# Kernel optimization log

Measured on AMD Instinct MI355X. Metric: run time of the kernel, lower is better.

## Reference

```python
import jax, jax.numpy as jnp
import numpy as np

N, E, W, H, NXF, NDF = 131072, 8, 128, 64, 10, 4
DX = 3 + 3 * 2 * NXF  # 63
DV = 3 + 3 * 2 * NDF  # 27
TEMP = 0.166667


def pe(x, degree):
    # positional encoding: [x, sin(2^i x), cos(2^i x)]
    y = jnp.concatenate([(2.0 ** i) * x for i in range(degree)], -1)
    return jnp.concatenate([x, jnp.sin(y), jnp.cos(y)], -1)


def setup_inputs() -> dict:
    key = jax.random.key(0)
    ks = jax.random.split(key, 8)
    s = 0.05
    return {
        'x': jax.random.normal(ks[0], (N, 6), jnp.float32),
        'W_enc': jax.random.normal(ks[1], (DX, W), jnp.float32) * s,
        'b_enc': jnp.zeros((W,), jnp.float32),
        'W_sh': jax.random.normal(ks[2], (E, W, W), jnp.float32) * s,
        'b_sh': jnp.zeros((E, W), jnp.float32),
        'w_sig': jax.random.normal(ks[3], (W,), jnp.float32) * s,
        'b_sig': jnp.zeros((1,), jnp.float32),
        'W_r1': jax.random.normal(ks[4], (E, W + DV, H), jnp.float32) * s,
        'b_r1': jnp.zeros((E, H), jnp.float32),
        'W_r2': jax.random.normal(ks[5], (E, H, 3), jnp.float32) * s,
        'b_r2': jnp.zeros((E, 3), jnp.float32),
    }


def reference(x, W_enc, b_enc, W_sh, b_sh, w_sig, b_sig, W_r1, b_r1, W_r2, b_r2):
    xyz = pe(x[:, :3], NXF)          # [N, 63]
    vd = pe(x[:, 3:6], NDF)          # [N, 27]
    y = jax.nn.relu(xyz @ W_enc + b_enc)  # encoding_xyz -> [N, W]
    # all shape experts at once: [N, E, W]
    shape_out = jax.nn.relu(jnp.einsum('nd,edh->neh', y, W_sh) + b_sh)
    # shared sigma head, softplus keeps sigma > 0: [N, E]
    sigmas = jax.nn.softplus(jnp.einsum('neh,h->ne', shape_out, w_sig) + b_sig)
    log_logits = jax.nn.log_softmax(jnp.log(sigmas + 1e-10) / TEMP, axis=-1)
    # gumbel-softmax (tau=1, torch default) with fixed noise key
    u = jax.random.uniform(jax.random.key(42), sigmas.shape, jnp.float32)
    g = -jnp.log(-jnp.log(u + 1e-20) + 1e-20)
    gates_soft = jax.nn.softmax(log_logits + g, axis=-1)
    index = jnp.argmax(gates_soft, axis=-1)  # [N]
    hard = jax.nn.one_hot(index, E, dtype=sigmas.dtype)
    # straight-through hard gates
    gates_hard = hard - jax.lax.stop_gradient(gates_soft) + gates_soft
    sigmas_pooled = jnp.take_along_axis(sigmas, index[:, None], axis=-1)  # [N, 1]
    # rgb experts: concat(shape_out_i, viewdir) -> MLP -> sigmoid rgb, gated sum
    vdb = jnp.broadcast_to(vd[:, None, :], (vd.shape[0], E, DV))
    inp = jnp.concatenate([shape_out, vdb], axis=-1)  # [N, E, W+27]
    h = jax.nn.relu(jnp.einsum('nec,ech->neh', inp, W_r1) + b_r1)
    rgb = jax.nn.sigmoid(jnp.einsum('neh,eho->neo', h, W_r2) + b_r2)  # [N, E, 3]
    rgbs = jnp.sum(rgb * gates_hard[:, :, None], axis=1)  # [N, 3]
    return jnp.concatenate([rgbs, sigmas_pooled], axis=-1)  # [N, 4]
```

## Files before the change

### kernel.cpp

```cpp
#include <hip/hip_runtime.h>
#include <hip/hip_bf16.h>


#define NPTS 131072
#define PT 64
#define NTH 256
#define NBLK (NPTS / PT)
#define INV2048 (1.0f / 2048.0f)

#define WS_ENC_H 0
#define WS_ENC_L 8192
#define WS_SH_H  16384
#define WS_SH_L  147456
#define WS_R1_H  278528

#define OFF_YH   0
#define OFF_B    17408
#define OFF_RED  38912
#define SMEM_SZ  47104

#define S_LIST(s) (*(int*)(smem + OFF_B + (s) * 336 + 320))
#define S_BID(p)  (*(int*)(smem + OFF_B + (p) * 336 + 324))
#define S_CNT(e)  (*(int*)(smem + OFF_B + (e) * 336 + 328))
#define S_OFF(e)  (*(int*)(smem + OFF_B + (e) * 336 + 332))

typedef __attribute__((ext_vector_type(8))) _Float16 f16x8;
typedef __attribute__((ext_vector_type(4))) _Float16 f16x4;
typedef __attribute__((ext_vector_type(4))) float f32x4;

#define MFMA(a, b, c) __builtin_amdgcn_mfma_f32_16x16x32_f16((a), (b), (c), 0, 0, 0)

__device__ __forceinline__ unsigned rotl32(unsigned x, int d) {
  return (x << d) | (x >> (32 - d));
}

__device__ __forceinline__ float gumbel_for(unsigned flat) {
  const unsigned k0 = 0u, k1 = 42u;
  const unsigned ks2 = k0 ^ k1 ^ 0x1BD11BDAu;
  unsigned x0 = 0u + k0;
  unsigned x1 = flat + k1;
#define TF_RND(r) { x0 += x1; x1 = rotl32(x1, r); x1 ^= x0; }
  TF_RND(13) TF_RND(15) TF_RND(26) TF_RND(6)
  x0 += k1;  x1 += ks2 + 1u;
  TF_RND(17) TF_RND(29) TF_RND(16) TF_RND(24)
  x0 += ks2; x1 += k0 + 2u;
  TF_RND(13) TF_RND(15) TF_RND(26) TF_RND(6)
  x0 += k0;  x1 += k1 + 3u;
  TF_RND(17) TF_RND(29) TF_RND(16) TF_RND(24)
  x0 += k1;  x1 += ks2 + 4u;
  TF_RND(13) TF_RND(15) TF_RND(26) TF_RND(6)
  x0 += ks2; x1 += k0 + 5u;
#undef TF_RND
  unsigned bits = x0 ^ x1;
  float u = __uint_as_float((bits >> 9) | 0x3f800000u) - 1.0f;
  return -logf(-logf(u + 1e-20f) + 1e-20f);
}

__global__ void prep_kernel(const float* __restrict__ W_enc,
                            const float* __restrict__ W_sh,
                            const float* __restrict__ W_r1,
                            _Float16* __restrict__ ws) {
  int idx = blockIdx.x * 256 + threadIdx.x;
  if (idx < 8192) {
    int tile = idx >> 9, r = idx & 511;
    int L = r >> 3, j = r & 7;
    int nt = tile >> 1, kt = tile & 1;
    int k = kt * 32 + (L >> 4) * 8 + j;
    int n = nt * 16 + (L & 15);
    float v = (k < 63) ? W_enc[k * 128 + n] : 0.0f;
    _Float16 h = (_Float16)v;
    ws[WS_ENC_H + idx] = h;
    ws[WS_ENC_L + idx] = (_Float16)((v - (float)h) * 2048.0f);
  } else if (idx < 8192 + 131072) {
    int s = idx - 8192;
    int tile = s >> 9, r = s & 511;
    int L = r >> 3, j = r & 7;
    int e = tile >> 5, nt = (tile >> 2) & 7, kt = tile & 3;
    int k = kt * 32 + (L >> 4) * 8 + j;
    int n = nt * 16 + (L & 15);
    float v = W_sh[e * 16384 + k * 128 + n];
    _Float16 h = (_Float16)v;
    ws[WS_SH_H + s] = h;
    ws[WS_SH_L + s] = (_Float16)((v - (float)h) * 2048.0f);
  } else if (idx < 8192 + 131072 + 81920) {
    int s = idx - (8192 + 131072);
    int tile = s >> 9, r = s & 511;
    int L = r >> 3, j = r & 7;
    int e = tile / 20, rr = tile % 20;
    int nt = rr / 5, kt = rr % 5;
    int k = kt * 32 + (L >> 4) * 8 + j;
    int n = nt * 16 + (L & 15);
    float v = (k < 155) ? W_r1[e * 9920 + k * 64 + n] : 0.0f;
    ws[WS_R1_H + s] = (_Float16)v;
  }
}

__global__ __launch_bounds__(NTH, 2)
void nerf_moe_kernel(const float* __restrict__ x,
                     const float* __restrict__ b_enc,
                     const float* __restrict__ b_sh,
                     const float* __restrict__ w_sig, const float* __restrict__ b_sig,
                     const float* __restrict__ b_r1,
                     const float* __restrict__ W_r2,  const float* __restrict__ b_r2,
                     const _Float16* __restrict__ wsw,
                     float* __restrict__ out) {
  __shared__ __align__(16) unsigned char smem[SMEM_SZ];
  _Float16* sYh  = (_Float16*)(smem + OFF_YH);
  float*    sH   = (float*)(smem + OFF_YH);
  _Float16* sYl  = (_Float16*)(smem + OFF_B);
  _Float16* sPEh = (_Float16*)(smem + OFF_B);
  _Float16* sPEl = (_Float16*)(smem + OFF_B + 9216);
  _Float16* sSB  = (_Float16*)(smem + OFF_B);
  float*    sRedE = (float*)(smem + OFF_RED);

  const int t  = threadIdx.x;
  const int w  = t >> 6;
  const int L  = t & 63;
  const int q  = L >> 4;
  const int c  = L & 15;
  const int n0 = blockIdx.x * PT;

  for (int idx = t; idx < PT * 64; idx += NTH) {
    int p = idx >> 6, f = idx & 63;
    const float* xr = x + (size_t)(n0 + p) * 6;
    float v;
    if (f < 3)       v = xr[f];
    else if (f < 33) { int g = f - 3;  v = sinf(xr[g % 3] * (float)(1 << (g / 3))); }
    else if (f < 63) { int g = f - 33; v = cosf(xr[g % 3] * (float)(1 << (g / 3))); }
    else             v = 0.0f;
    _Float16 h = (_Float16)v;
    sPEh[p * 72 + f] = h;
    sPEl[p * 72 + f] = (_Float16)((v - (float)h) * 2048.0f);
  }
  __syncthreads();

  {
    f16x8 beh[2][2], bel[2][2];
    #pragma unroll
    for (int ntL = 0; ntL < 2; ++ntL)
      #pragma unroll
      for (int kt = 0; kt < 2; ++kt) {
        int tile = (2 * w + ntL) * 2 + kt;
        beh[ntL][kt] = *(const f16x8*)(wsw + WS_ENC_H + tile * 512 + L * 8);
        bel[ntL][kt] = *(const f16x8*)(wsw + WS_ENC_L + tile * 512 + L * 8);
      }
    f16x8 pah[4][2], pal[4][2];
    #pragma unroll
    for (int mt = 0; mt < 4; ++mt)
      #pragma unroll
      for (int kt = 0; kt < 2; ++kt) {
        int off = (mt * 16 + c) * 72 + kt * 32 + q * 8;
        pah[mt][kt] = *(const f16x8*)(sPEh + off);
        pal[mt][kt] = *(const f16x8*)(sPEl + off);
      }
    f32x4 a1[4][2], a2[4][2];
    #pragma unroll
    for (int mt = 0; mt < 4; ++mt)
      #pragma unroll
      for (int ntL = 0; ntL < 2; ++ntL) { a1[mt][ntL] = (f32x4)0.0f; a2[mt][ntL] = (f32x4)0.0f; }
    #pragma unroll
    for (int kt = 0; kt < 2; ++kt)
      #pragma unroll
      for (int mt = 0; mt < 4; ++mt)
        #pragma unroll
        for (int ntL = 0; ntL < 2; ++ntL) {
          a1[mt][ntL] = MFMA(pah[mt][kt], beh[ntL][kt], a1[mt][ntL]);
          a2[mt][ntL] = MFMA(pah[mt][kt], bel[ntL][kt], a2[mt][ntL]);
          a2[mt][ntL] = MFMA(pal[mt][kt], beh[ntL][kt], a2[mt][ntL]);
        }
    __syncthreads();
    float bb0 = b_enc[(2 * w) * 16 + c];
    float bb1 = b_enc[(2 * w + 1) * 16 + c];
    #pragma unroll
    for (int mt = 0; mt < 4; ++mt)
      #pragma unroll
      for (int ntL = 0; ntL < 2; ++ntL) {
        float bb = ntL ? bb1 : bb0;
        int col = (2 * w + ntL) * 16 + c;
        #pragma unroll
        for (int r = 0; r < 4; ++r) {
          float v = fmaxf(a1[mt][ntL][r] + a2[mt][ntL][r] * INV2048 + bb, 0.0f);
          int row = mt * 16 + q * 4 + r;
          _Float16 h = (_Float16)v;
          sYh[row * 136 + col] = h;
          sYl[row * 136 + col] = (_Float16)((v - (float)h) * 2048.0f);
        }
      }
  }
  __syncthreads();

  f16x8 Ah[4][4];
  #pragma unroll
  for (int nt = 0; nt < 4; ++nt)
    #pragma unroll
    for (int kt = 0; kt < 4; ++kt)
      Ah[nt][kt] = *(const f16x8*)(sYh + (nt * 16 + c) * 136 + kt * 32 + q * 8);
  const f32x4 wsv0 = *(const f32x4*)(w_sig + (2 * w) * 16 + q * 4);
  const f32x4 wsv1 = *(const f32x4*)(w_sig + (2 * w + 1) * 16 + q * 4);

  float psum[4] = {0.f, 0.f, 0.f, 0.f};

  auto LOADW = [&](int s, f16x8 bh[4], f16x8 bl[4], f32x4& bb) {
    int e = s >> 1, i = s & 1;
    int tbase = (e * 8 + 2 * w + i) * 4;
    #pragma unroll
    for (int kt = 0; kt < 4; ++kt) {
      bh[kt] = *(const f16x8*)(wsw + WS_SH_H + (tbase + kt) * 512 + L * 8);
      bl[kt] = *(const f16x8*)(wsw + WS_SH_L + (tbase + kt) * 512 + L * 8);
    }
    bb = *(const f32x4*)(b_sh + e * 128 + (2 * w + i) * 16 + q * 4);
  };

  auto STEP = [&](int s, const f16x8 bh[4], const f16x8 bl[4], const f32x4& bb) {
    f32x4 a1[4], a2[4];
    #pragma unroll
    for (int nt = 0; nt < 4; ++nt) { a1[nt] = (f32x4)0.0f; a2[nt] = (f32x4)0.0f; }
    #pragma unroll
    for (int kt = 0; kt < 4; ++kt)
      #pragma unroll
      for (int nt = 0; nt < 4; ++nt) {
        f16x8 al = *(const f16x8*)(sYl + (nt * 16 + c) * 136 + kt * 32 + q * 8);
        a1[nt] = MFMA(bh[kt], Ah[nt][kt], a1[nt]);
        a2[nt] = MFMA(bl[kt], Ah[nt][kt], a2[nt]);
        a2[nt] = MFMA(bh[kt], al, a2[nt]);
      }
    f32x4 wv = (s & 1) ? wsv1 : wsv0;
    #pragma unroll
    for (int nt = 0; nt < 4; ++nt)
      #pragma unroll
      for (int r = 0; r < 4; ++r) {
        float sv = fmaxf(fmaf(a2[nt][r], INV2048, a1[nt][r]) + bb[r], 0.0f);
        psum[nt] = fmaf(sv, wv[r], psum[nt]);
      }
    if (s & 1) {
      int e = s >> 1;
      #pragma unroll
      for (int nt = 0; nt < 4; ++nt) {
        float v = psum[nt];
        v += __shfl_xor(v, 16);
        v += __shfl_xor(v, 32);
        if (q == 0) sRedE[e * 256 + w * 64 + nt * 16 + c] = v;
        psum[nt] = 0.f;
      }
    }
  };

  {
    f16x8 bh0[4], bl0[4], bh1[4], bl1[4];
    f32x4 bb0, bb1;
    LOADW(0, bh0, bl0, bb0);
    #pragma unroll
    for (int s = 0; s < 16; ++s) {
      if ((s & 1) == 0) {
        if (s + 1 < 16) LOADW(s + 1, bh1, bl1, bb1);
        STEP(s, bh0, bl0, bb0);
      } else {
        if (s + 1 < 16) LOADW(s + 1, bh0, bl0, bb0);
        STEP(s, bh1, bl1, bb1);
      }
    }
  }
  __syncthreads();

  {
    int pt = t >> 2;
    int eb = (t & 3) * 2;
    float best = -1e30f, bsig = 0.0f;
    int bide = 0;
    const float bs = b_sig[0];
    #pragma unroll
    for (int j = 0; j < 2; ++j) {
      int e = eb + j;
      const float* rp = sRedE + e * 256 + pt;
      float s = (rp[0] + rp[64]) + (rp[128] + rp[192]);
      float dotv = s + bs;
      float sig = fmaxf(dotv, 0.0f) + log1pf(expf(-fabsf(dotv)));
      float z = logf(sig + 1e-10f) / 0.166667f;
      float score = z + gumbel_for((unsigned)((n0 + pt) * 8 + e));
      if (score > best) { best = score; bsig = sig; bide = e; }
    }
    #pragma unroll
    for (int m = 1; m <= 2; m <<= 1) {
      float oS  = __shfl_xor(best, m);
      float oSg = __shfl_xor(bsig, m);
      int   oI  = __shfl_xor(bide, m);
      if (oS > best || (oS == best && oI < bide)) { best = oS; bsig = oSg; bide = oI; }
    }
    if ((t & 3) == 0) {
      S_BID(pt) = bide;
      out[(size_t)(n0 + pt) * 4 + 3] = bsig;
    }
  }
  __syncthreads();

  if (t < 8) {
    int cnt = 0;
    for (int p = 0; p < PT; ++p) cnt += (S_BID(p) == t);
    S_CNT(t) = cnt;
  }
  __syncthreads();
  if (t < 8) {
    int off = 0;
    for (int i = 0; i < t; ++i) off += S_CNT(i);
    S_OFF(t) = off;
    int k = off;
    for (int p = 0; p < PT; ++p) if (S_BID(p) == t) { S_LIST(k) = p; k++; }
  }
  __syncthreads();

  for (int idx = t; idx < PT * 32; idx += NTH) {
    int s = idx >> 5, cc = idx & 31;
    int pt = S_LIST(s);
    const float* xr = x + (size_t)(n0 + pt) * 6 + 3;
    float v;
    if (cc < 3)       v = xr[cc];
    else if (cc < 15) { int g = cc - 3;  v = sinf(xr[g % 3] * (float)(1 << (g / 3))); }
    else if (cc < 27) { int g = cc - 15; v = cosf(xr[g % 3] * (float)(1 << (g / 3))); }
    else              v = 0.0f;
    sSB[s * 168 + 128 + cc] = (_Float16)v;
  }
  #pragma unroll 1
  for (int ei = 0; ei < 2; ++ei) {
    int e = 2 * w + ei;
    int cnt = S_CNT(e), off = S_OFF(e);
    for (int base = 0; base < cnt; base += 16) {
      int sidx = base + c; if (sidx >= cnt) sidx = cnt - 1;
      int pt = S_LIST(off + sidx);
      f16x8 yb[4];
      #pragma unroll
      for (int kt = 0; kt < 4; ++kt)
        yb[kt] = *(const f16x8*)(sYh + pt * 136 + kt * 32 + q * 8);
      f32x4 acc[8];
      #pragma unroll
      for (int jt = 0; jt < 8; ++jt) acc[jt] = (f32x4)0.0f;
      #pragma unroll
      for (int jt = 0; jt < 8; ++jt)
        #pragma unroll
        for (int kt = 0; kt < 4; ++kt) {
          f16x8 a = *(const f16x8*)(wsw + WS_SH_H + ((e * 8 + jt) * 4 + kt) * 512 + L * 8);
          acc[jt] = MFMA(a, yb[kt], acc[jt]);
        }
      bool wr = (base + c) < cnt;
      int slot = off + base + c;
      #pragma unroll
      for (int jt = 0; jt < 8; ++jt) {
        f32x4 bb = *(const f32x4*)(b_sh + e * 128 + jt * 16 + q * 4);
        f16x4 v;
        #pragma unroll
        for (int r = 0; r < 4; ++r)
          v[r] = (_Float16)fmaxf(acc[jt][r] + bb[r], 0.0f);
        if (wr) *(f16x4*)(sSB + slot * 168 + jt * 16 + q * 4) = v;
      }
    }
  }
  __syncthreads();

  #pragma unroll 1
  for (int ei = 0; ei < 2; ++ei) {
    int e = 2 * w + ei;
    int cnt = S_CNT(e), off = S_OFF(e);
    for (int base = 0; base < cnt; base += 16) {
      int sidx = base + c; if (sidx >= cnt) sidx = cnt - 1;
      int slot = off + sidx;
      f16x8 ag[5];
      #pragma unroll
      for (int kt = 0; kt < 5; ++kt)
        ag[kt] = *(const f16x8*)(sSB + slot * 168 + kt * 32 + q * 8);
      f32x4 hacc[4];
      #pragma unroll
      for (int nt = 0; nt < 4; ++nt) hacc[nt] = (f32x4)0.0f;
      #pragma unroll
      for (int nt = 0; nt < 4; ++nt)
        #pragma unroll
        for (int kt = 0; kt < 5; ++kt) {
          f16x8 bf = *(const f16x8*)(wsw + WS_R1_H + ((e * 4 + nt) * 5 + kt) * 512 + L * 8);
          hacc[nt] = MFMA(ag[kt], bf, hacc[nt]);
        }
      #pragma unroll
      for (int nt = 0; nt < 4; ++nt) {
        float bb = b_r1[e * 64 + nt * 16 + c];
        #pragma unroll
        for (int r = 0; r < 4; ++r) {
          int m = q * 4 + r;
          if (base + m < cnt)
            sH[(off + base + m) * 68 + nt * 16 + c] = fmaxf(hacc[nt][r] + bb, 0.0f);
        }
      }
    }
  }
  __syncthreads();

  if (t < 192) {
    int s = t / 3, o = t - s * 3;
    int pt = S_LIST(s);
    int e = S_BID(pt);
    float a = b_r2[e * 3 + o];
    const float* w2 = W_r2 + e * 192 + o;
    #pragma unroll
    for (int jj = 0; jj < 64; jj += 4) {
      f32x4 h4 = *(const f32x4*)(sH + s * 68 + jj);
      a = fmaf(h4.x, w2[jj * 3], a);
      a = fmaf(h4.y, w2[jj * 3 + 3], a);
      a = fmaf(h4.z, w2[jj * 3 + 6], a);
      a = fmaf(h4.w, w2[jj * 3 + 9], a);
    }
    out[(size_t)(n0 + pt) * 4 + o] = 1.0f / (1.0f + expf(-a));
  }
}

extern "C" void kernel_launch(void* const* d_in, const int* in_sizes, int n_in,
                              void* d_out, int out_size, void* d_ws, size_t ws_size,
                              hipStream_t stream) {
  (void)in_sizes; (void)n_in; (void)ws_size; (void)out_size;
  const float* x     = (const float*)d_in[0];
  const float* W_enc = (const float*)d_in[1];
  const float* b_enc = (const float*)d_in[2];
  const float* W_sh  = (const float*)d_in[3];
  const float* b_sh  = (const float*)d_in[4];
  const float* w_sig = (const float*)d_in[5];
  const float* b_sig = (const float*)d_in[6];
  const float* W_r1  = (const float*)d_in[7];
  const float* b_r1  = (const float*)d_in[8];
  const float* W_r2  = (const float*)d_in[9];
  const float* b_r2  = (const float*)d_in[10];
  _Float16* ws = (_Float16*)d_ws;
  float* outp = (float*)d_out;
  prep_kernel<<<864, 256, 0, stream>>>(W_enc, W_sh, W_r1, ws);
  nerf_moe_kernel<<<NBLK, NTH, 0, stream>>>(x, b_enc, b_sh, w_sig, b_sig,
                                            b_r1, W_r2, b_r2, ws, outp);
}
```

Baseline: 278.3 us.

## Cut register pressure to raise occupancy to three blocks per CU

Raises launch bounds from 2 to 3 blocks per SM. The encoder GEMM is remapped so each wave owns 16 points across all hidden columns, with encoder weights streamed from global memory per tile instead of held in registers. The shape-expert loop now reloads the high-part Y fragments from LDS on every step instead of keeping a 4x4 register array of them. This lowers register use to fit the tighter bound, at the cost of more LDS reads and global weight loads, plus a risk of spills.

```diff
diff --git a/kernel.cpp b/kernel.cpp
--- a/kernel.cpp
+++ b/kernel.cpp
@@ -95,7 +95,7 @@
   }
 }
 
-__global__ __launch_bounds__(NTH, 2)
+__global__ __launch_bounds__(NTH, 3)
 void nerf_moe_kernel(const float* __restrict__ x,
                      const float* __restrict__ b_enc,
                      const float* __restrict__ b_sh,
@@ -135,66 +135,46 @@
   __syncthreads();
 
   {
-    f16x8 beh[2][2], bel[2][2];
-    #pragma unroll
-    for (int ntL = 0; ntL < 2; ++ntL)
-      #pragma unroll
-      for (int kt = 0; kt < 2; ++kt) {
-        int tile = (2 * w + ntL) * 2 + kt;
-        beh[ntL][kt] = *(const f16x8*)(wsw + WS_ENC_H + tile * 512 + L * 8);
-        bel[ntL][kt] = *(const f16x8*)(wsw + WS_ENC_L + tile * 512 + L * 8);
-      }
-    f16x8 pah[4][2], pal[4][2];
-    #pragma unroll
-    for (int mt = 0; mt < 4; ++mt)
-      #pragma unroll
-      for (int kt = 0; kt < 2; ++kt) {
-        int off = (mt * 16 + c) * 72 + kt * 32 + q * 8;
-        pah[mt][kt] = *(const f16x8*)(sPEh + off);
-        pal[mt][kt] = *(const f16x8*)(sPEl + off);
-      }
-    f32x4 a1[4][2], a2[4][2];
-    #pragma unroll
-    for (int mt = 0; mt < 4; ++mt)
-      #pragma unroll
-      for (int ntL = 0; ntL < 2; ++ntL) { a1[mt][ntL] = (f32x4)0.0f; a2[mt][ntL] = (f32x4)0.0f; }
-    #pragma unroll
-    for (int kt = 0; kt < 2; ++kt)
-      #pragma unroll
-      for (int mt = 0; mt < 4; ++mt)
-        #pragma unroll
-        for (int ntL = 0; ntL < 2; ++ntL) {
-          a1[mt][ntL] = MFMA(pah[mt][kt], beh[ntL][kt], a1[mt][ntL]);
-          a2[mt][ntL] = MFMA(pah[mt][kt], bel[ntL][kt], a2[mt][ntL]);
-          a2[mt][ntL] = MFMA(pal[mt][kt], beh[ntL][kt], a2[mt][ntL]);
+    f16x8 peh[2], pel[2];
+    #pragma unroll
+    for (int kt = 0; kt < 2; ++kt) {
+      peh[kt] = *(const f16x8*)(sPEh + (w * 16 + c) * 72 + kt * 32 + q * 8);
+      pel[kt] = *(const f16x8*)(sPEl + (w * 16 + c) * 72 + kt * 32 + q * 8);
+    }
+    __syncthreads();
+    #pragma unroll
+    for (int half = 0; half < 2; ++half) {
+      f32x4 a1[4], a2[4];
+      #pragma unroll
+      for (int ht = 0; ht < 4; ++ht) { a1[ht] = (f32x4)0.0f; a2[ht] = (f32x4)0.0f; }
+      #pragma unroll
+      for (int ht = 0; ht < 4; ++ht) {
+        int hT = half * 4 + ht;
+        #pragma unroll
+        for (int kt = 0; kt < 2; ++kt) {
+          f16x8 beh = *(const f16x8*)(wsw + WS_ENC_H + (hT * 2 + kt) * 512 + L * 8);
+          f16x8 bel = *(const f16x8*)(wsw + WS_ENC_L + (hT * 2 + kt) * 512 + L * 8);
+          a1[ht] = MFMA(beh, peh[kt], a1[ht]);
+          a2[ht] = MFMA(bel, peh[kt], a2[ht]);
+          a2[ht] = MFMA(beh, pel[kt], a2[ht]);
         }
-    __syncthreads();
-    float bb0 = b_enc[(2 * w) * 16 + c];
-    float bb1 = b_enc[(2 * w + 1) * 16 + c];
-    #pragma unroll
-    for (int mt = 0; mt < 4; ++mt)
-      #pragma unroll
-      for (int ntL = 0; ntL < 2; ++ntL) {
-        float bb = ntL ? bb1 : bb0;
-        int col = (2 * w + ntL) * 16 + c;
+      }
+      #pragma unroll
+      for (int ht = 0; ht < 4; ++ht) {
+        f32x4 bbv = *(const f32x4*)(b_enc + (half * 4 + ht) * 16 + q * 4);
         #pragma unroll
         for (int r = 0; r < 4; ++r) {
-          float v = fmaxf(a1[mt][ntL][r] + a2[mt][ntL][r] * INV2048 + bb, 0.0f);
-          int row = mt * 16 + q * 4 + r;
+          int hidx = (half * 4 + ht) * 16 + q * 4 + r;
+          float v = fmaxf(a1[ht][r] + a2[ht][r] * INV2048 + bbv[r], 0.0f);
           _Float16 h = (_Float16)v;
-          sYh[row * 136 + col] = h;
-          sYl[row * 136 + col] = (_Float16)((v - (float)h) * 2048.0f);
+          sYh[(w * 16 + c) * 136 + hidx] = h;
+          sYl[(w * 16 + c) * 136 + hidx] = (_Float16)((v - (float)h) * 2048.0f);
         }
       }
-  }
-  __syncthreads();
-
-  f16x8 Ah[4][4];
-  #pragma unroll
-  for (int nt = 0; nt < 4; ++nt)
-    #pragma unroll
-    for (int kt = 0; kt < 4; ++kt)
-      Ah[nt][kt] = *(const f16x8*)(sYh + (nt * 16 + c) * 136 + kt * 32 + q * 8);
+    }
+  }
+  __syncthreads();
+
   const f32x4 wsv0 = *(const f32x4*)(w_sig + (2 * w) * 16 + q * 4);
   const f32x4 wsv1 = *(const f32x4*)(w_sig + (2 * w + 1) * 16 + q * 4);
 
@@ -219,10 +199,11 @@
     for (int kt = 0; kt < 4; ++kt)
       #pragma unroll
       for (int nt = 0; nt < 4; ++nt) {
-        f16x8 al = *(const f16x8*)(sYl + (nt * 16 + c) * 136 + kt * 32 + q * 8);
-        a1[nt] = MFMA(bh[kt], Ah[nt][kt], a1[nt]);
-        a2[nt] = MFMA(bl[kt], Ah[nt][kt], a2[nt]);
-        a2[nt] = MFMA(bh[kt], al, a2[nt]);
+        f16x8 yh = *(const f16x8*)(sYh + (nt * 16 + c) * 136 + kt * 32 + q * 8);
+        f16x8 yl = *(const f16x8*)(sYl + (nt * 16 + c) * 136 + kt * 32 + q * 8);
+        a1[nt] = MFMA(bh[kt], yh, a1[nt]);
+        a2[nt] = MFMA(bl[kt], yh, a2[nt]);
+        a2[nt] = MFMA(bh[kt], yl, a2[nt]);
       }
     f32x4 wv = (s & 1) ? wsv1 : wsv0;
     #pragma unroll
```

Result: slower. 353.6 us (+27.1%).

## Use single-fp16 shape GEMM for gating, recompute near-ties in fp32

Applied to the files above, without the earlier changes.

Drops the split hi/lo fp16 compensation for the W_sh gating pass, so only one MFMA per tile runs instead of three and the lo-weight loads and workspace writes disappear. To keep the argmax exact, each point tracks its top-two gumbel scores. Points whose margin falls below a fixed tolerance get their eight expert sigmas recomputed in full fp32 from the original W_sh, and the selection is redone. Small index arrays move to a dedicated shared-memory region. The risk is that the tolerance may not cover the fp16 error, and the fp32 fallback is slow and divergent if many points are flagged.

```diff
diff --git a/kernel.cpp b/kernel.cpp
--- a/kernel.cpp
+++ b/kernel.cpp
@@ -7,22 +7,18 @@
 #define NTH 256
 #define NBLK (NPTS / PT)
 #define INV2048 (1.0f / 2048.0f)
+#define TAU 0.02f
 
 #define WS_ENC_H 0
 #define WS_ENC_L 8192
 #define WS_SH_H  16384
-#define WS_SH_L  147456
 #define WS_R1_H  278528
 
-#define OFF_YH   0
-#define OFF_B    17408
-#define OFF_RED  38912
-#define SMEM_SZ  47104
-
-#define S_LIST(s) (*(int*)(smem + OFF_B + (s) * 336 + 320))
-#define S_BID(p)  (*(int*)(smem + OFF_B + (p) * 336 + 324))
-#define S_CNT(e)  (*(int*)(smem + OFF_B + (e) * 336 + 328))
-#define S_OFF(e)  (*(int*)(smem + OFF_B + (e) * 336 + 332))
+#define OFF_YH    0
+#define OFF_B     17408
+#define OFF_RED   38912
+#define OFF_SMALL 47104
+#define SMEM_SZ   47680
 
 typedef __attribute__((ext_vector_type(8))) _Float16 f16x8;
 typedef __attribute__((ext_vector_type(4))) _Float16 f16x4;
@@ -54,6 +50,10 @@
   unsigned bits = x0 ^ x1;
   float u = __uint_as_float((bits >> 9) | 0x3f800000u) - 1.0f;
   return -logf(-logf(u + 1e-20f) + 1e-20f);
+}
+
+__device__ __forceinline__ float softplus_f(float dotv) {
+  return fmaxf(dotv, 0.0f) + log1pf(expf(-fabsf(dotv)));
 }
 
 __global__ void prep_kernel(const float* __restrict__ W_enc,
@@ -78,10 +78,7 @@
     int e = tile >> 5, nt = (tile >> 2) & 7, kt = tile & 3;
     int k = kt * 32 + (L >> 4) * 8 + j;
     int n = nt * 16 + (L & 15);
-    float v = W_sh[e * 16384 + k * 128 + n];
-    _Float16 h = (_Float16)v;
-    ws[WS_SH_H + s] = h;
-    ws[WS_SH_L + s] = (_Float16)((v - (float)h) * 2048.0f);
+    ws[WS_SH_H + s] = (_Float16)W_sh[e * 16384 + k * 128 + n];
   } else if (idx < 8192 + 131072 + 81920) {
     int s = idx - (8192 + 131072);
     int tile = s >> 9, r = s & 511;
@@ -98,6 +95,7 @@
 __global__ __launch_bounds__(NTH, 2)
 void nerf_moe_kernel(const float* __restrict__ x,
                      const float* __restrict__ b_enc,
+                     const float* __restrict__ W_sh,
                      const float* __restrict__ b_sh,
                      const float* __restrict__ w_sig, const float* __restrict__ b_sig,
                      const float* __restrict__ b_r1,
@@ -112,6 +110,11 @@
   _Float16* sPEl = (_Float16*)(smem + OFF_B + 9216);
   _Float16* sSB  = (_Float16*)(smem + OFF_B);
   float*    sRedE = (float*)(smem + OFF_RED);
+  int*      sSm  = (int*)(smem + OFF_SMALL);
+#define IBID(p)  sSm[(p)]
+#define ILIST(s) sSm[64 + (s)]
+#define ICNT(e)  sSm[128 + (e)]
+#define IOFF(e)  sSm[136 + (e)]
 
   const int t  = threadIdx.x;
   const int w  = t >> 6;
@@ -197,39 +200,34 @@
       Ah[nt][kt] = *(const f16x8*)(sYh + (nt * 16 + c) * 136 + kt * 32 + q * 8);
   const f32x4 wsv0 = *(const f32x4*)(w_sig + (2 * w) * 16 + q * 4);
   const f32x4 wsv1 = *(const f32x4*)(w_sig + (2 * w + 1) * 16 + q * 4);
+  const float bs = b_sig[0];
 
   float psum[4] = {0.f, 0.f, 0.f, 0.f};
 
-  auto LOADW = [&](int s, f16x8 bh[4], f16x8 bl[4], f32x4& bb) {
+  auto LOADW = [&](int s, f16x8 bh[4], f32x4& bb) {
     int e = s >> 1, i = s & 1;
     int tbase = (e * 8 + 2 * w + i) * 4;
     #pragma unroll
-    for (int kt = 0; kt < 4; ++kt) {
+    for (int kt = 0; kt < 4; ++kt)
       bh[kt] = *(const f16x8*)(wsw + WS_SH_H + (tbase + kt) * 512 + L * 8);
-      bl[kt] = *(const f16x8*)(wsw + WS_SH_L + (tbase + kt) * 512 + L * 8);
-    }
     bb = *(const f32x4*)(b_sh + e * 128 + (2 * w + i) * 16 + q * 4);
   };
 
-  auto STEP = [&](int s, const f16x8 bh[4], const f16x8 bl[4], const f32x4& bb) {
-    f32x4 a1[4], a2[4];
-    #pragma unroll
-    for (int nt = 0; nt < 4; ++nt) { a1[nt] = (f32x4)0.0f; a2[nt] = (f32x4)0.0f; }
+  auto STEP = [&](int s, const f16x8 bh[4], const f32x4& bb) {
+    f32x4 a1[4];
+    #pragma unroll
+    for (int nt = 0; nt < 4; ++nt) a1[nt] = (f32x4)0.0f;
     #pragma unroll
     for (int kt = 0; kt < 4; ++kt)
       #pragma unroll
-      for (int nt = 0; nt < 4; ++nt) {
-        f16x8 al = *(const f16x8*)(sYl + (nt * 16 + c) * 136 + kt * 32 + q * 8);
+      for (int nt = 0; nt < 4; ++nt)
         a1[nt] = MFMA(bh[kt], Ah[nt][kt], a1[nt]);
-        a2[nt] = MFMA(bl[kt], Ah[nt][kt], a2[nt]);
-        a2[nt] = MFMA(bh[kt], al, a2[nt]);
-      }
     f32x4 wv = (s & 1) ? wsv1 : wsv0;
     #pragma unroll
     for (int nt = 0; nt < 4; ++nt)
       #pragma unroll
       for (int r = 0; r < 4; ++r) {
-        float sv = fmaxf(fmaf(a2[nt][r], INV2048, a1[nt][r]) + bb[r], 0.0f);
+        float sv = fmaxf(a1[nt][r] + bb[r], 0.0f);
         psum[nt] = fmaf(sv, wv[r], psum[nt]);
       }
     if (s & 1) {
@@ -246,17 +244,17 @@
   };
 
   {
-    f16x8 bh0[4], bl0[4], bh1[4], bl1[4];
+    f16x8 bh0[4], bh1[4];
     f32x4 bb0, bb1;
-    LOADW(0, bh0, bl0, bb0);
+    LOADW(0, bh0, bb0);
     #pragma unroll
     for (int s = 0; s < 16; ++s) {
       if ((s & 1) == 0) {
-        if (s + 1 < 16) LOADW(s + 1, bh1, bl1, bb1);
-        STEP(s, bh0, bl0, bb0);
+        if (s + 1 < 16) LOADW(s + 1, bh1, bb1);
+        STEP(s, bh0, bb0);
       } else {
-        if (s + 1 < 16) LOADW(s + 1, bh0, bl0, bb0);
-        STEP(s, bh1, bl1, bb1);
+        if (s + 1 < 16) LOADW(s + 1, bh0, bb0);
+        STEP(s, bh1, bb1);
       }
     }
   }
@@ -265,52 +263,102 @@
   {
     int pt = t >> 2;
     int eb = (t & 3) * 2;
-    float best = -1e30f, bsig = 0.0f;
-    int bide = 0;
-    const float bs = b_sig[0];
+    float s_[2], sg_[2];
     #pragma unroll
     for (int j = 0; j < 2; ++j) {
       int e = eb + j;
       const float* rp = sRedE + e * 256 + pt;
       float s = (rp[0] + rp[64]) + (rp[128] + rp[192]);
-      float dotv = s + bs;
-      float sig = fmaxf(dotv, 0.0f) + log1pf(expf(-fabsf(dotv)));
+      float sig = softplus_f(s + bs);
       float z = logf(sig + 1e-10f) / 0.166667f;
-      float score = z + gumbel_for((unsigned)((n0 + pt) * 8 + e));
-      if (score > best) { best = score; bsig = sig; bide = e; }
-    }
+      s_[j] = z + gumbel_for((unsigned)((n0 + pt) * 8 + e));
+      sg_[j] = sig;
+    }
+    float T1s, T2s, T1g; int T1i;
+    if (s_[1] > s_[0]) { T1s = s_[1]; T1i = eb + 1; T1g = sg_[1]; T2s = s_[0]; }
+    else               { T1s = s_[0]; T1i = eb;     T1g = sg_[0]; T2s = s_[1]; }
     #pragma unroll
     for (int m = 1; m <= 2; m <<= 1) {
-      float oS  = __shfl_xor(best, m);
-      float oSg = __shfl_xor(bsig, m);
-      int   oI  = __shfl_xor(bide, m);
-      if (oS > best || (oS == best && oI < bide)) { best = oS; bsig = oSg; bide = oI; }
-    }
+      float oS = __shfl_xor(T1s, m);
+      int   oI = __shfl_xor(T1i, m);
+      float oG = __shfl_xor(T1g, m);
+      float o2 = __shfl_xor(T2s, m);
+      bool ow = (oS > T1s) || (oS == T1s && oI < T1i);
+      float n2 = ow ? fmaxf(T1s, o2) : fmaxf(oS, T2s);
+      if (ow) { T1s = oS; T1i = oI; T1g = oG; }
+      T2s = n2;
+    }
+    float myBid = (float)T1i, myBsig = T1g;
+    int   myBidI = T1i;
+    bool flg = (T1s - T2s) < TAU;
+    unsigned long long bl = __ballot(flg);
+
+    unsigned m16 = 0;
+    #pragma unroll
+    for (int k = 0; k < 16; ++k)
+      m16 |= ((unsigned)((bl >> (4 * k)) & 1ull)) << k;
+    while (m16) {
+      int kloc = (int)__builtin_ctz(m16);
+      m16 &= m16 - 1;
+      int ptf = (w << 4) | kloc;
+      int e2 = L >> 3, seg = L & 7;
+      float S[16];
+      #pragma unroll
+      for (int jj = 0; jj < 16; ++jj) S[jj] = 0.0f;
+      const float* Wp = W_sh + e2 * 16384 + seg * 16;
+      for (int k = 0; k < 128; ++k) {
+        float yk = (float)sYh[ptf * 136 + k] + (float)sYl[ptf * 136 + k] * INV2048;
+        const float* wr = Wp + k * 128;
+        #pragma unroll
+        for (int jj = 0; jj < 16; ++jj)
+          S[jj] = fmaf(yk, wr[jj], S[jj]);
+      }
+      float part = 0.0f;
+      #pragma unroll
+      for (int jj = 0; jj < 16; ++jj) {
+        float sv = fmaxf(S[jj] + b_sh[e2 * 128 + seg * 16 + jj], 0.0f);
+        part = fmaf(sv, w_sig[seg * 16 + jj], part);
+      }
+      part += __shfl_xor(part, 1);
+      part += __shfl_xor(part, 2);
+      part += __shfl_xor(part, 4);
+      float best = 0.f, bsg = 0.f; int bid = 0;
+      #pragma unroll
+      for (int e3 = 0; e3 < 8; ++e3) {
+        float dote = __shfl(part, e3 * 8);
+        float sig = softplus_f(dote + bs);
+        float z = logf(sig + 1e-10f) / 0.166667f;
+        float score = z + gumbel_for((unsigned)((n0 + ptf) * 8 + e3));
+        if (e3 == 0 || score > best) { best = score; bsg = sig; bid = e3; }
+      }
+      if (L == (kloc << 2)) { myBidI = bid; myBsig = bsg; }
+    }
+    (void)myBid;
     if ((t & 3) == 0) {
-      S_BID(pt) = bide;
-      out[(size_t)(n0 + pt) * 4 + 3] = bsig;
+      IBID(pt) = myBidI;
+      out[(size_t)(n0 + pt) * 4 + 3] = myBsig;
     }
   }
   __syncthreads();
 
   if (t < 8) {
     int cnt = 0;
-    for (int p = 0; p < PT; ++p) cnt += (S_BID(p) == t);
-    S_CNT(t) = cnt;
+    for (int p = 0; p < PT; ++p) cnt += (IBID(p) == t);
+    ICNT(t) = cnt;
   }
   __syncthreads();
   if (t < 8) {
     int off = 0;
-    for (int i = 0; i < t; ++i) off += S_CNT(i);
-    S_OFF(t) = off;
+    for (int i = 0; i < t; ++i) off += ICNT(i);
+    IOFF(t) = off;
     int k = off;
-    for (int p = 0; p < PT; ++p) if (S_BID(p) == t) { S_LIST(k) = p; k++; }
+    for (int p = 0; p < PT; ++p) if (IBID(p) == t) { ILIST(k) = p; k++; }
   }
   __syncthreads();
 
   for (int idx = t; idx < PT * 32; idx += NTH) {
     int s = idx >> 5, cc = idx & 31;
-    int pt = S_LIST(s);
+    int pt = ILIST(s);
     const float* xr = x + (size_t)(n0 + pt) * 6 + 3;
     float v;
     if (cc < 3)       v = xr[cc];
@@ -322,10 +370,10 @@
   #pragma unroll 1
   for (int ei = 0; ei < 2; ++ei) {
     int e = 2 * w + ei;
-    int cnt = S_CNT(e), off = S_OFF(e);
+    int cnt = ICNT(e), off = IOFF(e);
     for (int base = 0; base < cnt; base += 16) {
       int sidx = base + c; if (sidx >= cnt) sidx = cnt - 1;
-      int pt = S_LIST(off + sidx);
+      int pt = ILIST(off + sidx);
       f16x8 yb[4];
       #pragma unroll
       for (int kt = 0; kt < 4; ++kt)
@@ -358,7 +406,7 @@
   #pragma unroll 1
   for (int ei = 0; ei < 2; ++ei) {
     int e = 2 * w + ei;
-    int cnt = S_CNT(e), off = S_OFF(e);
+    int cnt = ICNT(e), off = IOFF(e);
     for (int base = 0; base < cnt; base += 16) {
       int sidx = base + c; if (sidx >= cnt) sidx = cnt - 1;
       int slot = off + sidx;
@@ -392,8 +440,8 @@
 
   if (t < 192) {
     int s = t / 3, o = t - s * 3;
-    int pt = S_LIST(s);
-    int e = S_BID(pt);
+    int pt = ILIST(s);
+    int e = IBID(pt);
     float a = b_r2[e * 3 + o];
     const float* w2 = W_r2 + e * 192 + o;
     #pragma unroll
@@ -406,6 +454,10 @@
     }
     out[(size_t)(n0 + pt) * 4 + o] = 1.0f / (1.0f + expf(-a));
   }
+#undef IBID
+#undef ILIST
+#undef ICNT
+#undef IOFF
 }
 
 extern "C" void kernel_launch(void* const* d_in, const int* in_sizes, int n_in,
@@ -426,6 +478,6 @@
   _Float16* ws = (_Float16*)d_ws;
   float* outp = (float*)d_out;
   prep_kernel<<<864, 256, 0, stream>>>(W_enc, W_sh, W_r1, ws);
-  nerf_moe_kernel<<<NBLK, NTH, 0, stream>>>(x, b_enc, b_sh, w_sig, b_sig,
+  nerf_moe_kernel<<<NBLK, NTH, 0, stream>>>(x, b_enc, W_sh, b_sh, w_sig, b_sig,
                                             b_r1, W_r2, b_r2, ws, outp);
 }
```

Result: slower. 367.7 us (+32.1%).
